# Kernel tuning notes

Hardware: AMD Instinct MI355X
Metric: run time of the kernel (lower is better)

## Reference

```python
import jax, jax.numpy as jnp
import numpy as np

NUM_USERS = 100000
NUM_ITEMS = 50000
N_NODES = NUM_USERS + NUM_ITEMS
NUM_COMMUNITY = 64
N_LAYERS = 3
NNZ = 2400000
BATCH = 8192
NEG_SLOPE = 0.1
EPS = 1e-12


def setup_inputs() -> dict:
    key = jax.random.key(0)
    ks = jax.random.split(key, 9)
    stdv = 1.0 / np.sqrt(NUM_COMMUNITY)
    return {
        "users": jax.random.randint(ks[0], (BATCH,), 0, NUM_USERS, dtype=jnp.int64 if jax.config.jax_enable_x64 else jnp.int32).astype(jnp.int32),
        "adjacent_items": jax.random.randint(ks[1], (BATCH,), 0, NUM_ITEMS).astype(jnp.int32),
        "weak_items": jax.random.randint(ks[2], (BATCH,), 0, NUM_ITEMS).astype(jnp.int32),
        "strong_items": jax.random.randint(ks[3], (BATCH,), 0, NUM_ITEMS).astype(jnp.int32),
        "edge_rows": jax.random.randint(ks[4], (NNZ,), 0, N_NODES).astype(jnp.int32),
        "edge_cols": jax.random.randint(ks[5], (NNZ,), 0, N_NODES).astype(jnp.int32),
        "edge_vals": jax.random.uniform(ks[6], (NNZ,), dtype=jnp.float32),
        "user_preference": jax.random.uniform(ks[7], (NUM_USERS, NUM_COMMUNITY), dtype=jnp.float32, minval=-stdv, maxval=stdv),
        "item_preference": jax.random.uniform(ks[8], (NUM_ITEMS, NUM_COMMUNITY), dtype=jnp.float32, minval=-stdv, maxval=stdv),
    }


def _lrelu_l2norm(x):
    # leaky_relu(neg_slope=0.1) then L2-normalize along last dim (torch F.normalize semantics)
    x = jnp.where(x >= 0, x, NEG_SLOPE * x)
    norm = jnp.sqrt(jnp.sum(x * x, axis=-1, keepdims=True))
    return x / jnp.maximum(norm, EPS)


def reference(users, adjacent_items, weak_items, strong_items,
              edge_rows, edge_cols, edge_vals,
              user_preference, item_preference):
    # ---- computer(): LightGCN-style propagation over sparse adjacency ----
    pref = _lrelu_l2norm(jnp.concatenate([user_preference, item_preference], axis=0))  # [N, C]
    acc = pref
    p = pref
    for _ in range(N_LAYERS):
        # sparse.mm(Graph, p): gather source rows, scale by edge values, scatter-add into dest rows
        msg = edge_vals[:, None] * p[edge_cols]                      # [nnz, C]
        p = jax.ops.segment_sum(msg, edge_rows, num_segments=N_NODES)  # [N, C]
        p = _lrelu_l2norm(p)
        acc = acc + p
    merged = acc / (N_LAYERS + 1)  # mean over stacked layers
    users_pref = merged[:NUM_USERS]
    items_pref = merged[NUM_USERS:]

    # ---- forward(): per-pair dot products + sigmoid ----
    u = users_pref[users]  # [B, C]

    def score(items):
        return jax.nn.sigmoid(jnp.sum(u * items_pref[items], axis=-1))

    # stack of (adjacent, weak, strong) gamma preferences, shape [3, B]
    return jnp.stack([score(adjacent_items), score(weak_items), score(strong_items)], axis=0)
```

## Files before the change

### kernel.cpp

```cpp
#include <hip/hip_runtime.h>
#include <math.h>

#define D 64
#define NUM_USERS 100000
#define NUM_ITEMS 50000
#define N_NODES 150000
#define NNZ 2400000
#define BATCH 8192
#define NEG_SLOPE 0.1f
#define EPS_NRM 1e-12f

#define NBUCKET 586
#define NCHUNK  256
#define CH      9376
#define NH      (NBUCKET * NCHUNK)
#define NBH     (NH / 256)
#define CAP     6144
#define VSCALE  16383.f

typedef unsigned short ushort_t;
typedef unsigned char  uchar_t;

__device__ __forceinline__ float wave_sum64(float v) {
    #pragma unroll
    for (int off = 32; off > 0; off >>= 1)
        v += __shfl_xor(v, off, 64);
    return v;
}

__device__ __forceinline__ int wave_sum64_i(int v) {
    #pragma unroll
    for (int off = 32; off > 0; off >>= 1)
        v += __shfl_xor(v, off, 64);
    return v;
}

__device__ __forceinline__ float bf2f(ushort_t u) {
    return __uint_as_float(((unsigned)u) << 16);
}
__device__ __forceinline__ ushort_t f2bf(float f) {
    unsigned x = __float_as_uint(f);
    unsigned r = (x + 0x7FFFu + ((x >> 16) & 1u)) >> 16;
    return (ushort_t)r;
}


__global__ void bucket_hist(const int* __restrict__ rows, int* __restrict__ ht) {
    __shared__ int hist[NBUCKET];
    int c = blockIdx.x, tid = threadIdx.x;
    for (int b = tid; b < NBUCKET; b += 256) hist[b] = 0;
    __syncthreads();
    int base = c * CH;
    int n = NNZ - base; if (n > CH) n = CH;
    const int4* r4 = (const int4*)(rows + base);
    for (int i = tid; i < (n >> 2); i += 256) {
        int4 r = r4[i];
        atomicAdd(&hist[r.x >> 8], 1);
        atomicAdd(&hist[r.y >> 8], 1);
        atomicAdd(&hist[r.z >> 8], 1);
        atomicAdd(&hist[r.w >> 8], 1);
    }
    __syncthreads();
    for (int b = tid; b < NBUCKET; b += 256) ht[b * NCHUNK + c] = hist[b];
}

__global__ void scan1_kernel(const int* __restrict__ in, int* __restrict__ out,
                             int* __restrict__ bsums, int n) {
    int tid = threadIdx.x, gid = blockIdx.x * 256 + tid;
    int v = (gid < n) ? in[gid] : 0;
    int lane = tid & 63, w = tid >> 6;
    int s = v;
    #pragma unroll
    for (int off = 1; off < 64; off <<= 1) {
        int t = __shfl_up(s, off, 64);
        if (lane >= off) s += t;
    }
    __shared__ int wsum[4];
    if (lane == 63) wsum[w] = s;
    __syncthreads();
    if (tid == 0) {
        int a = 0;
        #pragma unroll
        for (int i = 0; i < 4; i++) { int t = wsum[i]; wsum[i] = a; a += t; }
    }
    __syncthreads();
    int incl = s + wsum[w];
    if (gid < n) out[gid] = incl - v;
    if (tid == 255) bsums[blockIdx.x] = incl;
}

__global__ void scan3_kernel(int* __restrict__ out, const int* __restrict__ bsums, int n) {
    __shared__ int wtot[4];
    __shared__ int total;
    int b = blockIdx.x, tid = threadIdx.x;
    int lane = tid & 63, w = tid >> 6;
    int partial = 0;
    for (int i = tid; i < b; i += 256) partial += bsums[i];
    partial = wave_sum64_i(partial);
    if (lane == 0) wtot[w] = partial;
    __syncthreads();
    if (tid == 0) total = wtot[0] + wtot[1] + wtot[2] + wtot[3];
    __syncthreads();
    int gid = b * 256 + tid;
    if (gid < n) out[gid] += total;
}

__global__ void __launch_bounds__(512) bucket_scatter(
        const int* __restrict__ rows, const int* __restrict__ cols,
        const float* __restrict__ vals, const int* __restrict__ hoff,
        unsigned* __restrict__ es4, uchar_t* __restrict__ rlow) {
    __shared__ int cur[NBUCKET];
    int c = blockIdx.x, tid = threadIdx.x;
    for (int b = tid; b < NBUCKET; b += 512) cur[b] = hoff[b * NCHUNK + c];
    __syncthreads();
    int base = c * CH;
    int n = NNZ - base; if (n > CH) n = CH;
    const int4*   r4 = (const int4*)(rows + base);
    const int4*   c4 = (const int4*)(cols + base);
    const float4* v4 = (const float4*)(vals + base);
    for (int i = tid; i < (n >> 2); i += 512) {
        int4 r = r4[i];
        int4 cc = c4[i];
        float4 v = v4[i];
        int p;
        p = atomicAdd(&cur[r.x >> 8], 1);
        es4[p] = (unsigned)cc.x | ((unsigned)(v.x * VSCALE + 0.5f) << 18);
        rlow[p] = (uchar_t)(r.x & 255);
        p = atomicAdd(&cur[r.y >> 8], 1);
        es4[p] = (unsigned)cc.y | ((unsigned)(v.y * VSCALE + 0.5f) << 18);
        rlow[p] = (uchar_t)(r.y & 255);
        p = atomicAdd(&cur[r.z >> 8], 1);
        es4[p] = (unsigned)cc.z | ((unsigned)(v.z * VSCALE + 0.5f) << 18);
        rlow[p] = (uchar_t)(r.z & 255);
        p = atomicAdd(&cur[r.w >> 8], 1);
        es4[p] = (unsigned)cc.w | ((unsigned)(v.w * VSCALE + 0.5f) << 18);
        rlow[p] = (uchar_t)(r.w & 255);
    }
}

__global__ void __launch_bounds__(1024) bucket_sort(const unsigned* __restrict__ es4,
                                                    const uchar_t* __restrict__ rlow,
                                                    const int* __restrict__ hoff,
                                                    unsigned* __restrict__ es,
                                                    int* __restrict__ rowptr) {
    __shared__ int      hist[256];
    __shared__ int      wsum[4];
    __shared__ unsigned outbuf[CAP];
    int b = blockIdx.x, tid = threadIdx.x;
    int beg = hoff[b * NCHUNK];
    int end = (b == NBUCKET - 1) ? NNZ : hoff[(b + 1) * NCHUNK];
    if (tid < 256) hist[tid] = 0;
    __syncthreads();
    for (int i = beg + tid; i < end; i += 1024)
        atomicAdd(&hist[rlow[i]], 1);
    __syncthreads();
    int excl = 0;
    if (tid < 256) {
        int v = hist[tid];
        int lane = tid & 63, w = tid >> 6;
        int s = v;
        #pragma unroll
        for (int off = 1; off < 64; off <<= 1) {
            int t = __shfl_up(s, off, 64);
            if (lane >= off) s += t;
        }
        if (lane == 63) wsum[w] = s;
        excl = s - v;
    }
    __syncthreads();
    if (tid == 0) {
        int a = 0;
        #pragma unroll
        for (int i = 0; i < 4; i++) { int t = wsum[i]; wsum[i] = a; a += t; }
    }
    __syncthreads();
    if (tid < 256) {
        excl += wsum[tid >> 6];
        int r = (b << 8) + tid;
        if (r <= N_NODES) rowptr[r] = beg + excl;
        hist[tid] = excl;
    }
    __syncthreads();
    for (int i = beg + tid; i < end; i += 1024) {
        int d = atomicAdd(&hist[rlow[i]], 1);
        outbuf[d] = es4[i];
    }
    __syncthreads();
    int n = end - beg;
    for (int i = tid; i < n; i += 1024)
        es[beg + i] = outbuf[i];
}

__global__ void init_kernel(const float* __restrict__ upref,
                            const float* __restrict__ ipref,
                            ushort_t* __restrict__ p0) {
    int row  = blockIdx.x * 4 + (threadIdx.x >> 6);
    int lane = threadIdx.x & 63;
    if (row >= N_NODES) return;
    float x = (row < NUM_USERS) ? upref[(size_t)row * D + lane]
                                : ipref[(size_t)(row - NUM_USERS) * D + lane];
    x = (x >= 0.f) ? x : NEG_SLOPE * x;
    float norm = sqrtf(wave_sum64(x * x));
    float y = x / fmaxf(norm, EPS_NRM);
    p0[(size_t)row * D + lane] = f2bf(y);
}

__global__ void gather_kernel(const int* __restrict__ rowptr,
                              const unsigned* __restrict__ es,
                              const ushort_t* __restrict__ p,
                              ushort_t* __restrict__ pn) {
    int row  = blockIdx.x * 4 + (threadIdx.x >> 6);
    int lane = threadIdx.x & 63;
    if (row >= N_NODES) return;
    int sub = lane >> 3;
    int fl  = lane & 7;
    int beg = rowptr[row], end = rowptr[row + 1];

    float a[8];
    #pragma unroll
    for (int k = 0; k < 8; k++) a[k] = 0.f;

    const float vs = 1.f / VSCALE;
    int e = beg + sub;
    while (e + 8 < end) {
        unsigned ev0 = es[e];
        unsigned ev1 = es[e + 8];
        const uint4 q0 = *(const uint4*)(p + (((ev0 & 0x3FFFFu) << 6) | (fl << 3)));
        const uint4 q1 = *(const uint4*)(p + (((ev1 & 0x3FFFFu) << 6) | (fl << 3)));
        float v0 = (float)(ev0 >> 18) * vs;
        float v1 = (float)(ev1 >> 18) * vs;
        a[0] = fmaf(v0, __uint_as_float(q0.x << 16),         a[0]);
        a[1] = fmaf(v0, __uint_as_float(q0.x & 0xFFFF0000u), a[1]);
        a[2] = fmaf(v0, __uint_as_float(q0.y << 16),         a[2]);
        a[3] = fmaf(v0, __uint_as_float(q0.y & 0xFFFF0000u), a[3]);
        a[4] = fmaf(v0, __uint_as_float(q0.z << 16),         a[4]);
        a[5] = fmaf(v0, __uint_as_float(q0.z & 0xFFFF0000u), a[5]);
        a[6] = fmaf(v0, __uint_as_float(q0.w << 16),         a[6]);
        a[7] = fmaf(v0, __uint_as_float(q0.w & 0xFFFF0000u), a[7]);
        a[0] = fmaf(v1, __uint_as_float(q1.x << 16),         a[0]);
        a[1] = fmaf(v1, __uint_as_float(q1.x & 0xFFFF0000u), a[1]);
        a[2] = fmaf(v1, __uint_as_float(q1.y << 16),         a[2]);
        a[3] = fmaf(v1, __uint_as_float(q1.y & 0xFFFF0000u), a[3]);
        a[4] = fmaf(v1, __uint_as_float(q1.z << 16),         a[4]);
        a[5] = fmaf(v1, __uint_as_float(q1.z & 0xFFFF0000u), a[5]);
        a[6] = fmaf(v1, __uint_as_float(q1.w << 16),         a[6]);
        a[7] = fmaf(v1, __uint_as_float(q1.w & 0xFFFF0000u), a[7]);
        e += 16;
    }
    if (e < end) {
        unsigned ev = es[e];
        const uint4 q = *(const uint4*)(p + (((ev & 0x3FFFFu) << 6) | (fl << 3)));
        float v = (float)(ev >> 18) * vs;
        a[0] = fmaf(v, __uint_as_float(q.x << 16),         a[0]);
        a[1] = fmaf(v, __uint_as_float(q.x & 0xFFFF0000u), a[1]);
        a[2] = fmaf(v, __uint_as_float(q.y << 16),         a[2]);
        a[3] = fmaf(v, __uint_as_float(q.y & 0xFFFF0000u), a[3]);
        a[4] = fmaf(v, __uint_as_float(q.z << 16),         a[4]);
        a[5] = fmaf(v, __uint_as_float(q.z & 0xFFFF0000u), a[5]);
        a[6] = fmaf(v, __uint_as_float(q.w << 16),         a[6]);
        a[7] = fmaf(v, __uint_as_float(q.w & 0xFFFF0000u), a[7]);
    }

    bool s0 = (sub & 1) != 0, s1 = (sub & 2) != 0, s2 = (sub & 4) != 0;
    float b[4];
    #pragma unroll
    for (int j = 0; j < 4; j++) {
        float send = s0 ? a[2 * j]     : a[2 * j + 1];
        float keep = s0 ? a[2 * j + 1] : a[2 * j];
        b[j] = keep + __shfl_xor(send, 8, 64);
    }
    float c[2];
    #pragma unroll
    for (int i = 0; i < 2; i++) {
        float send = s1 ? b[2 * i]     : b[2 * i + 1];
        float keep = s1 ? b[2 * i + 1] : b[2 * i];
        c[i] = keep + __shfl_xor(send, 16, 64);
    }
    float y;
    {
        float send = s2 ? c[0] : c[1];
        float keep = s2 ? c[1] : c[0];
        y = keep + __shfl_xor(send, 32, 64);
    }

    y = (y >= 0.f) ? y : NEG_SLOPE * y;
    float ss = wave_sum64(y * y);
    float inv = 1.f / fmaxf(sqrtf(ss), EPS_NRM);
    pn[(size_t)row * D + fl * 8 + sub] = f2bf(y * inv);
}

__global__ void score_kernel(const int* __restrict__ users,
                             const int* __restrict__ it0,
                             const int* __restrict__ it1,
                             const int* __restrict__ it2,
                             const ushort_t* __restrict__ p0,
                             const ushort_t* __restrict__ p1,
                             const ushort_t* __restrict__ p2,
                             const ushort_t* __restrict__ p3,
                             float* __restrict__ out) {
    int b    = blockIdx.x * 4 + (threadIdx.x >> 6);
    int lane = threadIdx.x & 63;
    if (b >= BATCH) return;
    int u = users[b];
    size_t uo = (size_t)u * D + lane;
    float uf = bf2f(p0[uo]) + bf2f(p1[uo]) + bf2f(p2[uo]) + bf2f(p3[uo]);

    int its[3];
    its[0] = it0[b]; its[1] = it1[b]; its[2] = it2[b];
    #pragma unroll
    for (int k = 0; k < 3; k++) {
        size_t io = (size_t)(NUM_USERS + its[k]) * D + lane;
        float itf = bf2f(p0[io]) + bf2f(p1[io]) + bf2f(p2[io]) + bf2f(p3[io]);
        float s = wave_sum64(uf * itf) * 0.0625f;
        if (lane == 0)
            out[k * BATCH + b] = 1.f / (1.f + expf(-s));
    }
}

extern "C" void kernel_launch(void* const* d_in, const int* in_sizes, int n_in,
                              void* d_out, int out_size, void* d_ws, size_t ws_size,
                              hipStream_t stream) {
    const int*   users  = (const int*)  d_in[0];
    const int*   adj    = (const int*)  d_in[1];
    const int*   weak   = (const int*)  d_in[2];
    const int*   strong = (const int*)  d_in[3];
    const int*   erows  = (const int*)  d_in[4];
    const int*   ecols  = (const int*)  d_in[5];
    const float* evals  = (const float*)d_in[6];
    const float* upref  = (const float*)d_in[7];
    const float* ipref  = (const float*)d_in[8];
    float* out = (float*)d_out;

    const size_t rowElems = (size_t)N_NODES * D;

    char* base = (char*)d_ws;
    size_t off = 0;
    auto alloc = [&](size_t bytes) {
        char* p = base + off;
        off = (off + bytes + 255) & ~(size_t)255;
        return (void*)p;
    };
    ushort_t* p0     = (ushort_t*)alloc(rowElems * sizeof(ushort_t));
    ushort_t* p1     = (ushort_t*)alloc(rowElems * sizeof(ushort_t));
    ushort_t* p2     = (ushort_t*)alloc(rowElems * sizeof(ushort_t));
    ushort_t* p3     = (ushort_t*)alloc(rowElems * sizeof(ushort_t));
    unsigned* es     = (unsigned*)alloc((size_t)NNZ * sizeof(unsigned));
    int*      ht     = (int*)     alloc((size_t)NH * sizeof(int));
    int*      hoff   = (int*)     alloc((size_t)NH * sizeof(int));
    int*      rowptr = (int*)     alloc((N_NODES + 1) * sizeof(int));
    int*      bsums  = (int*)     alloc(1024 * sizeof(int));
    unsigned* es4t   = (unsigned*)p2;
    uchar_t*  rlowt  = (uchar_t*)((char*)p2 + (size_t)NNZ * 4);

    bucket_hist   <<<NCHUNK, 256, 0, stream>>>(erows, ht);
    scan1_kernel  <<<NBH, 256, 0, stream>>>(ht, hoff, bsums, NH);
    scan3_kernel  <<<NBH, 256, 0, stream>>>(hoff, bsums, NH);
    bucket_scatter<<<NCHUNK, 512, 0, stream>>>(erows, ecols, evals, hoff, es4t, rlowt);
    bucket_sort   <<<NBUCKET, 1024, 0, stream>>>(es4t, rlowt, hoff, es, rowptr);

    init_kernel<<<(N_NODES + 3) / 4, 256, 0, stream>>>(upref, ipref, p0);
    gather_kernel<<<(N_NODES + 3) / 4, 256, 0, stream>>>(rowptr, es, p0, p1);
    gather_kernel<<<(N_NODES + 3) / 4, 256, 0, stream>>>(rowptr, es, p1, p2);
    gather_kernel<<<(N_NODES + 3) / 4, 256, 0, stream>>>(rowptr, es, p2, p3);

    score_kernel<<<(BATCH + 3) / 4, 256, 0, stream>>>(users, adj, weak, strong,
                                                      p0, p1, p2, p3, out);
}
```

Baseline: 382.9 us.

## Switch embeddings to fp16 and halve bucket count to 512 rows per bucket

Stores the propagated embedding tables in fp16 instead of bf16 and converts with hardware half-to-float conversions in the gather and score kernels. It also coarsens the CSR-building bucket sort from 256 to 512 rows per bucket, halving the histogram/scan size and the number of sort blocks, with 16-bit row offsets and a larger shared output buffer. The aim is to cut preprocessing launch and scan overhead and use cheaper conversions, with fp16 trading range for precision. The larger shared buffer may lower occupancy in the sort kernel, and a bucket holding more than 10240 edges would overflow it.

After: 372.7 us. 2.6% less time.

```diff
diff --git a/kernel.cpp b/kernel.cpp
--- a/kernel.cpp
+++ b/kernel.cpp
@@ -1,4 +1,5 @@
 #include <hip/hip_runtime.h>
+#include <hip/hip_fp16.h>
 #include <math.h>
 
 #define D 64
@@ -10,16 +11,16 @@
 #define NEG_SLOPE 0.1f
 #define EPS_NRM 1e-12f
 
-#define NBUCKET 586
+#define NB2     293
+#define RPB     512
 #define NCHUNK  256
 #define CH      9376
-#define NH      (NBUCKET * NCHUNK)
-#define NBH     (NH / 256)
-#define CAP     6144
+#define NHT     (NB2 * NCHUNK)
+#define NBH     (NHT / 256)
+#define CAP     10240
 #define VSCALE  16383.f
 
 typedef unsigned short ushort_t;
-typedef unsigned char  uchar_t;
 
 __device__ __forceinline__ float wave_sum64(float v) {
     #pragma unroll
@@ -35,33 +36,31 @@
     return v;
 }
 
-__device__ __forceinline__ float bf2f(ushort_t u) {
-    return __uint_as_float(((unsigned)u) << 16);
-}
-__device__ __forceinline__ ushort_t f2bf(float f) {
-    unsigned x = __float_as_uint(f);
-    unsigned r = (x + 0x7FFFu + ((x >> 16) & 1u)) >> 16;
-    return (ushort_t)r;
+__device__ __forceinline__ float h2f_lo(unsigned u) {
+    return __half2float(__ushort_as_half((unsigned short)(u & 0xFFFFu)));
+}
+__device__ __forceinline__ float h2f_hi(unsigned u) {
+    return __half2float(__ushort_as_half((unsigned short)(u >> 16)));
 }
 
 
 __global__ void bucket_hist(const int* __restrict__ rows, int* __restrict__ ht) {
-    __shared__ int hist[NBUCKET];
+    __shared__ int hist[NB2];
     int c = blockIdx.x, tid = threadIdx.x;
-    for (int b = tid; b < NBUCKET; b += 256) hist[b] = 0;
+    for (int b = tid; b < NB2; b += 256) hist[b] = 0;
     __syncthreads();
     int base = c * CH;
     int n = NNZ - base; if (n > CH) n = CH;
     const int4* r4 = (const int4*)(rows + base);
     for (int i = tid; i < (n >> 2); i += 256) {
         int4 r = r4[i];
-        atomicAdd(&hist[r.x >> 8], 1);
-        atomicAdd(&hist[r.y >> 8], 1);
-        atomicAdd(&hist[r.z >> 8], 1);
-        atomicAdd(&hist[r.w >> 8], 1);
-    }
-    __syncthreads();
-    for (int b = tid; b < NBUCKET; b += 256) ht[b * NCHUNK + c] = hist[b];
+        atomicAdd(&hist[r.x >> 9], 1);
+        atomicAdd(&hist[r.y >> 9], 1);
+        atomicAdd(&hist[r.z >> 9], 1);
+        atomicAdd(&hist[r.w >> 9], 1);
+    }
+    __syncthreads();
+    for (int b = tid; b < NB2; b += 256) ht[b * NCHUNK + c] = hist[b];
 }
 
 __global__ void scan1_kernel(const int* __restrict__ in, int* __restrict__ out,
@@ -108,10 +107,10 @@
 __global__ void __launch_bounds__(512) bucket_scatter(
         const int* __restrict__ rows, const int* __restrict__ cols,
         const float* __restrict__ vals, const int* __restrict__ hoff,
-        unsigned* __restrict__ es4, uchar_t* __restrict__ rlow) {
-    __shared__ int cur[NBUCKET];
+        unsigned* __restrict__ es4, ushort_t* __restrict__ rlow) {
+    __shared__ int cur[NB2];
     int c = blockIdx.x, tid = threadIdx.x;
-    for (int b = tid; b < NBUCKET; b += 512) cur[b] = hoff[b * NCHUNK + c];
+    for (int b = tid; b < NB2; b += 512) cur[b] = hoff[b * NCHUNK + c];
     __syncthreads();
     int base = c * CH;
     int n = NNZ - base; if (n > CH) n = CH;
@@ -123,39 +122,39 @@
         int4 cc = c4[i];
         float4 v = v4[i];
         int p;
-        p = atomicAdd(&cur[r.x >> 8], 1);
+        p = atomicAdd(&cur[r.x >> 9], 1);
         es4[p] = (unsigned)cc.x | ((unsigned)(v.x * VSCALE + 0.5f) << 18);
-        rlow[p] = (uchar_t)(r.x & 255);
-        p = atomicAdd(&cur[r.y >> 8], 1);
+        rlow[p] = (ushort_t)(r.x & (RPB - 1));
+        p = atomicAdd(&cur[r.y >> 9], 1);
         es4[p] = (unsigned)cc.y | ((unsigned)(v.y * VSCALE + 0.5f) << 18);
-        rlow[p] = (uchar_t)(r.y & 255);
-        p = atomicAdd(&cur[r.z >> 8], 1);
+        rlow[p] = (ushort_t)(r.y & (RPB - 1));
+        p = atomicAdd(&cur[r.z >> 9], 1);
         es4[p] = (unsigned)cc.z | ((unsigned)(v.z * VSCALE + 0.5f) << 18);
-        rlow[p] = (uchar_t)(r.z & 255);
-        p = atomicAdd(&cur[r.w >> 8], 1);
+        rlow[p] = (ushort_t)(r.z & (RPB - 1));
+        p = atomicAdd(&cur[r.w >> 9], 1);
         es4[p] = (unsigned)cc.w | ((unsigned)(v.w * VSCALE + 0.5f) << 18);
-        rlow[p] = (uchar_t)(r.w & 255);
+        rlow[p] = (ushort_t)(r.w & (RPB - 1));
     }
 }
 
 __global__ void __launch_bounds__(1024) bucket_sort(const unsigned* __restrict__ es4,
-                                                    const uchar_t* __restrict__ rlow,
+                                                    const ushort_t* __restrict__ rlow,
                                                     const int* __restrict__ hoff,
                                                     unsigned* __restrict__ es,
                                                     int* __restrict__ rowptr) {
-    __shared__ int      hist[256];
-    __shared__ int      wsum[4];
+    __shared__ int      hist[RPB];
+    __shared__ int      wsum[8];
     __shared__ unsigned outbuf[CAP];
     int b = blockIdx.x, tid = threadIdx.x;
     int beg = hoff[b * NCHUNK];
-    int end = (b == NBUCKET - 1) ? NNZ : hoff[(b + 1) * NCHUNK];
-    if (tid < 256) hist[tid] = 0;
+    int end = (b == NB2 - 1) ? NNZ : hoff[(b + 1) * NCHUNK];
+    if (tid < RPB) hist[tid] = 0;
     __syncthreads();
     for (int i = beg + tid; i < end; i += 1024)
         atomicAdd(&hist[rlow[i]], 1);
     __syncthreads();
     int excl = 0;
-    if (tid < 256) {
+    if (tid < RPB) {
         int v = hist[tid];
         int lane = tid & 63, w = tid >> 6;
         int s = v;
@@ -171,12 +170,12 @@
     if (tid == 0) {
         int a = 0;
         #pragma unroll
-        for (int i = 0; i < 4; i++) { int t = wsum[i]; wsum[i] = a; a += t; }
-    }
-    __syncthreads();
-    if (tid < 256) {
+        for (int i = 0; i < 8; i++) { int t = wsum[i]; wsum[i] = a; a += t; }
+    }
+    __syncthreads();
+    if (tid < RPB) {
         excl += wsum[tid >> 6];
-        int r = (b << 8) + tid;
+        int r = b * RPB + tid;
         if (r <= N_NODES) rowptr[r] = beg + excl;
         hist[tid] = excl;
     }
@@ -193,7 +192,7 @@
 
 __global__ void init_kernel(const float* __restrict__ upref,
                             const float* __restrict__ ipref,
-                            ushort_t* __restrict__ p0) {
+                            __half* __restrict__ p0) {
     int row  = blockIdx.x * 4 + (threadIdx.x >> 6);
     int lane = threadIdx.x & 63;
     if (row >= N_NODES) return;
@@ -202,13 +201,24 @@
     x = (x >= 0.f) ? x : NEG_SLOPE * x;
     float norm = sqrtf(wave_sum64(x * x));
     float y = x / fmaxf(norm, EPS_NRM);
-    p0[(size_t)row * D + lane] = f2bf(y);
+    p0[(size_t)row * D + lane] = __float2half(y);
+}
+
+__device__ __forceinline__ void acc8(float a[8], float v, uint4 q) {
+    a[0] = fmaf(v, h2f_lo(q.x), a[0]);
+    a[1] = fmaf(v, h2f_hi(q.x), a[1]);
+    a[2] = fmaf(v, h2f_lo(q.y), a[2]);
+    a[3] = fmaf(v, h2f_hi(q.y), a[3]);
+    a[4] = fmaf(v, h2f_lo(q.z), a[4]);
+    a[5] = fmaf(v, h2f_hi(q.z), a[5]);
+    a[6] = fmaf(v, h2f_lo(q.w), a[6]);
+    a[7] = fmaf(v, h2f_hi(q.w), a[7]);
 }
 
 __global__ void gather_kernel(const int* __restrict__ rowptr,
                               const unsigned* __restrict__ es,
-                              const ushort_t* __restrict__ p,
-                              ushort_t* __restrict__ pn) {
+                              const __half* __restrict__ p,
+                              __half* __restrict__ pn) {
     int row  = blockIdx.x * 4 + (threadIdx.x >> 6);
     int lane = threadIdx.x & 63;
     if (row >= N_NODES) return;
@@ -229,36 +239,15 @@
         const uint4 q1 = *(const uint4*)(p + (((ev1 & 0x3FFFFu) << 6) | (fl << 3)));
         float v0 = (float)(ev0 >> 18) * vs;
         float v1 = (float)(ev1 >> 18) * vs;
-        a[0] = fmaf(v0, __uint_as_float(q0.x << 16),         a[0]);
-        a[1] = fmaf(v0, __uint_as_float(q0.x & 0xFFFF0000u), a[1]);
-        a[2] = fmaf(v0, __uint_as_float(q0.y << 16),         a[2]);
-        a[3] = fmaf(v0, __uint_as_float(q0.y & 0xFFFF0000u), a[3]);
-        a[4] = fmaf(v0, __uint_as_float(q0.z << 16),         a[4]);
-        a[5] = fmaf(v0, __uint_as_float(q0.z & 0xFFFF0000u), a[5]);
-        a[6] = fmaf(v0, __uint_as_float(q0.w << 16),         a[6]);
-        a[7] = fmaf(v0, __uint_as_float(q0.w & 0xFFFF0000u), a[7]);
-        a[0] = fmaf(v1, __uint_as_float(q1.x << 16),         a[0]);
-        a[1] = fmaf(v1, __uint_as_float(q1.x & 0xFFFF0000u), a[1]);
-        a[2] = fmaf(v1, __uint_as_float(q1.y << 16),         a[2]);
-        a[3] = fmaf(v1, __uint_as_float(q1.y & 0xFFFF0000u), a[3]);
-        a[4] = fmaf(v1, __uint_as_float(q1.z << 16),         a[4]);
-        a[5] = fmaf(v1, __uint_as_float(q1.z & 0xFFFF0000u), a[5]);
-        a[6] = fmaf(v1, __uint_as_float(q1.w << 16),         a[6]);
-        a[7] = fmaf(v1, __uint_as_float(q1.w & 0xFFFF0000u), a[7]);
+        acc8(a, v0, q0);
+        acc8(a, v1, q1);
         e += 16;
     }
     if (e < end) {
         unsigned ev = es[e];
         const uint4 q = *(const uint4*)(p + (((ev & 0x3FFFFu) << 6) | (fl << 3)));
         float v = (float)(ev >> 18) * vs;
-        a[0] = fmaf(v, __uint_as_float(q.x << 16),         a[0]);
-        a[1] = fmaf(v, __uint_as_float(q.x & 0xFFFF0000u), a[1]);
-        a[2] = fmaf(v, __uint_as_float(q.y << 16),         a[2]);
-        a[3] = fmaf(v, __uint_as_float(q.y & 0xFFFF0000u), a[3]);
-        a[4] = fmaf(v, __uint_as_float(q.z << 16),         a[4]);
-        a[5] = fmaf(v, __uint_as_float(q.z & 0xFFFF0000u), a[5]);
-        a[6] = fmaf(v, __uint_as_float(q.w << 16),         a[6]);
-        a[7] = fmaf(v, __uint_as_float(q.w & 0xFFFF0000u), a[7]);
+        acc8(a, v, q);
     }
 
     bool s0 = (sub & 1) != 0, s1 = (sub & 2) != 0, s2 = (sub & 4) != 0;
@@ -286,31 +275,33 @@
     y = (y >= 0.f) ? y : NEG_SLOPE * y;
     float ss = wave_sum64(y * y);
     float inv = 1.f / fmaxf(sqrtf(ss), EPS_NRM);
-    pn[(size_t)row * D + fl * 8 + sub] = f2bf(y * inv);
+    pn[(size_t)row * D + fl * 8 + sub] = __float2half(y * inv);
 }
 
 __global__ void score_kernel(const int* __restrict__ users,
                              const int* __restrict__ it0,
                              const int* __restrict__ it1,
                              const int* __restrict__ it2,
-                             const ushort_t* __restrict__ p0,
-                             const ushort_t* __restrict__ p1,
-                             const ushort_t* __restrict__ p2,
-                             const ushort_t* __restrict__ p3,
+                             const __half* __restrict__ p0,
+                             const __half* __restrict__ p1,
+                             const __half* __restrict__ p2,
+                             const __half* __restrict__ p3,
                              float* __restrict__ out) {
     int b    = blockIdx.x * 4 + (threadIdx.x >> 6);
     int lane = threadIdx.x & 63;
     if (b >= BATCH) return;
     int u = users[b];
     size_t uo = (size_t)u * D + lane;
-    float uf = bf2f(p0[uo]) + bf2f(p1[uo]) + bf2f(p2[uo]) + bf2f(p3[uo]);
+    float uf = __half2float(p0[uo]) + __half2float(p1[uo])
+             + __half2float(p2[uo]) + __half2float(p3[uo]);
 
     int its[3];
     its[0] = it0[b]; its[1] = it1[b]; its[2] = it2[b];
     #pragma unroll
     for (int k = 0; k < 3; k++) {
         size_t io = (size_t)(NUM_USERS + its[k]) * D + lane;
-        float itf = bf2f(p0[io]) + bf2f(p1[io]) + bf2f(p2[io]) + bf2f(p3[io]);
+        float itf = __half2float(p0[io]) + __half2float(p1[io])
+                  + __half2float(p2[io]) + __half2float(p3[io]);
         float s = wave_sum64(uf * itf) * 0.0625f;
         if (lane == 0)
             out[k * BATCH + b] = 1.f / (1.f + expf(-s));
@@ -340,23 +331,23 @@
         off = (off + bytes + 255) & ~(size_t)255;
         return (void*)p;
     };
-    ushort_t* p0     = (ushort_t*)alloc(rowElems * sizeof(ushort_t));
-    ushort_t* p1     = (ushort_t*)alloc(rowElems * sizeof(ushort_t));
-    ushort_t* p2     = (ushort_t*)alloc(rowElems * sizeof(ushort_t));
-    ushort_t* p3     = (ushort_t*)alloc(rowElems * sizeof(ushort_t));
+    __half*   p0     = (__half*)  alloc(rowElems * sizeof(__half));
+    __half*   p1     = (__half*)  alloc(rowElems * sizeof(__half));
+    __half*   p2     = (__half*)  alloc(rowElems * sizeof(__half));
+    __half*   p3     = (__half*)  alloc(rowElems * sizeof(__half));
     unsigned* es     = (unsigned*)alloc((size_t)NNZ * sizeof(unsigned));
-    int*      ht     = (int*)     alloc((size_t)NH * sizeof(int));
-    int*      hoff   = (int*)     alloc((size_t)NH * sizeof(int));
-    int*      rowptr = (int*)     alloc((N_NODES + 1) * sizeof(int));
+    int*      ht     = (int*)     alloc((size_t)NHT * sizeof(int));
+    int*      hoff   = (int*)     alloc((size_t)NHT * sizeof(int));
+    int*      rowptr = (int*)     alloc((N_NODES + 2) * sizeof(int));
     int*      bsums  = (int*)     alloc(1024 * sizeof(int));
     unsigned* es4t   = (unsigned*)p2;
-    uchar_t*  rlowt  = (uchar_t*)((char*)p2 + (size_t)NNZ * 4);
+    ushort_t* rlowt  = (ushort_t*)((char*)p2 + (size_t)NNZ * 4);
 
     bucket_hist   <<<NCHUNK, 256, 0, stream>>>(erows, ht);
-    scan1_kernel  <<<NBH, 256, 0, stream>>>(ht, hoff, bsums, NH);
-    scan3_kernel  <<<NBH, 256, 0, stream>>>(hoff, bsums, NH);
+    scan1_kernel  <<<NBH, 256, 0, stream>>>(ht, hoff, bsums, NHT);
+    scan3_kernel  <<<NBH, 256, 0, stream>>>(hoff, bsums, NHT);
     bucket_scatter<<<NCHUNK, 512, 0, stream>>>(erows, ecols, evals, hoff, es4t, rlowt);
-    bucket_sort   <<<NBUCKET, 1024, 0, stream>>>(es4t, rlowt, hoff, es, rowptr);
+    bucket_sort   <<<NB2, 1024, 0, stream>>>(es4t, rlowt, hoff, es, rowptr);
 
     init_kernel<<<(N_NODES + 3) / 4, 256, 0, stream>>>(upref, ipref, p0);
     gather_kernel<<<(N_NODES + 3) / 4, 256, 0, stream>>>(rowptr, es, p0, p1);
```
